# Kernel optimization log

Hardware: AMD Instinct MI355X
Metric: run time of the kernel (lower is better)

## Reference

```python
import jax, jax.numpy as jnp
import numpy as np

ROI = (8, 8)          # local window (kh, kw)
H = 768
W = 768
C = ROI[0] * ROI[1]   # 64 channels == prod(roi), required by the local conv
N_LAYERS = 4          # n_decoder_layers
LN_EPS = 1e-6         # flax.linen.LayerNorm default


def setup_inputs() -> dict:
    key = jax.random.key(0)
    k0, k1, k2 = jax.random.split(key, 3)
    x = jax.random.normal(k0, (H, W, C), jnp.float32)  # post-FPN feature map
    Ws = jax.random.normal(k1, (N_LAYERS, C, C), jnp.float32) / np.float32(np.sqrt(C))
    bs = jnp.zeros((N_LAYERS, C), jnp.float32)
    ln_scale = jnp.ones((N_LAYERS, C), jnp.float32)
    ln_bias = jnp.zeros((N_LAYERS, C), jnp.float32)
    w_out = jax.random.normal(k2, (C, 1), jnp.float32) / np.float32(np.sqrt(C))
    b_out = jnp.zeros((1,), jnp.float32)
    return {"x": x, "Ws": Ws, "bs": bs, "ln_scale": ln_scale,
            "ln_bias": ln_bias, "w_out": w_out, "b_out": b_out}


def att(x, weights):
    # out[i,j,c] = sum_{di,dj} xpad[i+di, j+dj, c] * weights[i, j, di*kw+dj]
    # Equivalent to the original per-channel lax.scan over
    # conv_general_dilated_local (window ordering row-major, 'same' padding),
    # but batched over all C channels at once via shifted-slice accumulation
    # instead of materializing the (H, W, 64, C) patch tensor.
    kh, kw = ROI
    pt, pb = (kh - 1) // 2, kh - 1 - (kh - 1) // 2  # 'SAME' pad for even kernel: (3, 4)
    pl, pr = (kw - 1) // 2, kw - 1 - (kw - 1) // 2
    xpad = jnp.pad(x, ((pt, pb), (pl, pr), (0, 0)))

    def body(acc, k):
        di = k // kw
        dj = k % kw
        patch = jax.lax.dynamic_slice(xpad, (di, dj, 0), (H, W, C))
        return acc + patch * weights[:, :, k][:, :, None], None

    acc, _ = jax.lax.scan(body, jnp.zeros_like(x), jnp.arange(kh * kw))
    return acc


def layer_norm(x, scale, bias):
    mu = jnp.mean(x, axis=-1, keepdims=True)
    var = jnp.mean(jnp.square(x - mu), axis=-1, keepdims=True)
    return (x - mu) * jax.lax.rsqrt(var + LN_EPS) * scale + bias


def reference(x, Ws, bs, ln_scale, ln_bias, w_out, b_out):
    weights = jax.nn.sigmoid(x)            # spatially-varying local-conv weights
    x0 = att(x, weights)                   # (H, W, C)
    for i in range(N_LAYERS):              # MLP decoder stack
        x0 = jax.nn.relu(x0 @ Ws[i] + bs[i])
        x0 = layer_norm(x0, ln_scale[i], ln_bias[i])
    out = x0 @ w_out + b_out               # (H, W, 1)
    return (x0, out)
```

## Files before the change

### kernel.cpp

```cpp
#include <hip/hip_runtime.h>
#include <hip/hip_bf16.h>


#define HH 768
#define WW 768
#define HWPX (HH*WW)

typedef __attribute__((ext_vector_type(8))) short short8;
typedef __attribute__((ext_vector_type(8))) _Float16 half8;
typedef __attribute__((ext_vector_type(4))) float f32x4;

union hcvt { _Float16 h; ushort u; };
__device__ __forceinline__ ushort f2h(float f) { hcvt c; c.h = (_Float16)f; return c.u; }
__device__ __forceinline__ float sigmoidf(float v) { return 1.f / (1.f + __expf(-v)); }

__device__ __forceinline__ int goff(int row, int g) {
  return (row << 8) + (((g & ~7) | ((g ^ row) & 7)) << 3);
}
__device__ __forceinline__ int eoff(int row, int k) {
  const int g = k >> 3;
  return (row << 8) + (((g & ~7) | ((g ^ row) & 7)) << 3) + (k & 7);
}

__global__ __launch_bounds__(256, 2)
void att_k1(const float* __restrict__ x, float* __restrict__ attf) {
  __shared__ __align__(16) ushort Mb[64 * 256];
  __shared__ __align__(16) ushort Xb[64 * 256];
  const int tid = threadIdx.x;
  const int lane = tid & 63, w = tid >> 6;
  const int l15 = lane & 15, lg = lane >> 4;

  {
    const short8 z8 = {0,0,0,0,0,0,0,0};
    #pragma unroll
    for (int i = 0; i < 8; ++i)
      *reinterpret_cast<short8*>(&Mb[(tid + i * 256) * 8]) = z8;
    if (tid < 128) {
      const int row = tid >> 1, g = 30 + (tid & 1);
      *reinterpret_cast<short8*>(&Xb[goff(row, g)]) = z8;
    }
  }

  const int b = blockIdx.x;
  const int tbase = (b & 7) * 1152 + (b >> 3) * 18;
  const int p  = w * 16 + l15;
  const int pr = p >> 3, pc = p & 7;
  const int cb = lg << 4;
  const int arow = w * 16 + l15;

  float4 cv[4];
  float Rv[4][8];
  float Lv[4][8];
  short8 rs[4];

  auto issue_loads = [&](int ti, int tj, bool fresh) {
    {
      const float* cp = x + ((size_t)((ti + pr) * WW + (tj + pc)) << 6) + cb;
      #pragma unroll
      for (int qd = 0; qd < 4; ++qd)
        cv[qd] = *reinterpret_cast<const float4*>(cp + qd * 4);
    }
    #pragma unroll
    for (int i = 0; i < 4; ++i) {
      const int r = w + 4 * i;
      if (r < 15) {
        const int gr = min(max(ti + r - 3, 0), HH - 1);
        const float* rowp = x + ((size_t)gr * WW << 6) + lane;
        #pragma unroll
        for (int s = 0; s < 8; ++s) {
          const int gc = min(max(tj + 5 + s, 0), WW - 1);
          Rv[i][s] = rowp[(size_t)gc << 6];
        }
        if (fresh) {
          #pragma unroll
          for (int s = 0; s < 8; ++s) {
            const int gc = min(max(tj - 3 + s, 0), WW - 1);
            Lv[i][s] = rowp[(size_t)gc << 6];
          }
        }
      }
    }
  };

  auto write_lds = [&](int ti, int tj, bool fresh) {
    #pragma unroll
    for (int qd = 0; qd < 4; ++qd) {
      const float vs[4] = {cv[qd].x, cv[qd].y, cv[qd].z, cv[qd].w};
      #pragma unroll
      for (int j = 0; j < 4; ++j) {
        const int ch = cb + qd * 4 + j;
        const int k = ((pr + (ch >> 3)) << 4) | (pc + (ch & 7));
        Mb[eoff(p, k)] = f2h(sigmoidf(vs[j]));
      }
    }
    #pragma unroll
    for (int i = 0; i < 4; ++i) {
      const int r = w + 4 * i;
      if (r < 15) {
        const int gr = ti + r - 3;
        const bool rok = (unsigned)gr < (unsigned)HH;
        short8 left8;
        if (fresh) {
          #pragma unroll
          for (int s = 0; s < 8; ++s) {
            const int j = tj - 3 + s;
            const bool ok = rok && ((unsigned)j < (unsigned)WW);
            left8[s] = (short)f2h(ok ? Lv[i][s] : 0.f);
          }
        } else {
          left8 = rs[i];
        }
        short8 right8;
        #pragma unroll
        for (int s = 0; s < 8; ++s) {
          const int j = tj + 5 + s;
          const bool ok = rok && ((unsigned)j < (unsigned)WW);
          right8[s] = (short)f2h(ok ? Rv[i][s] : 0.f);
        }
        *reinterpret_cast<short8*>(&Xb[goff(lane, 2 * r)])     = left8;
        *reinterpret_cast<short8*>(&Xb[goff(lane, 2 * r + 1)]) = right8;
        rs[i] = right8;
      }
    }
  };

  {
    const int t0 = tbase;
    issue_loads((t0 / 96) * 8, (t0 % 96) * 8, true);
  }

  for (int t18 = 0; t18 < 18; ++t18) {
    const int tile = tbase + t18;
    const int ti = (tile / 96) * 8, tj = (tile % 96) * 8;
    const bool fresh = (t18 == 0) || (tj == 0);

    __syncthreads();
    write_lds(ti, tj, fresh);
    __syncthreads();

    if (t18 < 17) {
      const int nt = tile + 1;
      issue_loads((nt / 96) * 8, (nt % 96) * 8, (nt % 96) == 0);
    }

    f32x4 acc[4];
    #pragma unroll
    for (int nb = 0; nb < 4; ++nb) acc[nb] = {0.f, 0.f, 0.f, 0.f};
    #pragma unroll
    for (int ks = 0; ks < 8; ++ks) {
      const int g = ks * 4 + lg;
      const half8 a = *reinterpret_cast<const half8*>(&Mb[goff(arow, g)]);
      #pragma unroll
      for (int nb = 0; nb < 4; ++nb) {
        const half8 bb = *reinterpret_cast<const half8*>(&Xb[goff(nb * 16 + l15, g)]);
        acc[nb] = __builtin_amdgcn_mfma_f32_16x16x32_f16(a, bb, acc[nb], 0, 0, 0);
      }
    }

    #pragma unroll
    for (int reg = 0; reg < 4; ++reg) {
      const int pl = w * 16 + lg * 4 + reg;
      const size_t gpx = (size_t)(ti + (pl >> 3)) * WW + (tj + (pl & 7));
      #pragma unroll
      for (int nb = 0; nb < 4; ++nb)
        attf[(gpx << 6) + nb * 16 + l15] = acc[nb][reg];
    }
  }
}

__global__ __launch_bounds__(512, 4)
void mlp_k2(const float* attf, const float* __restrict__ Ws,
            const float* __restrict__ bs, const float* __restrict__ lns,
            const float* __restrict__ lnb, const float* __restrict__ w_out,
            const float* __restrict__ b_out, float* x0_out,
            float* __restrict__ out1) {
  __shared__ __align__(16) ushort wt[4 * 64 * 64];
  __shared__ __align__(16) ushort act[8 * 1152];
  const int tid = threadIdx.x;
  const int lane = tid & 63, wid = tid >> 6;
  const int l15 = lane & 15, lg = lane >> 4;

  {
    const int row = tid >> 1;
    const int l = row >> 6, co = row & 63;
    const int ci0 = (tid & 1) << 5;
    const int base = row << 6;
    for (int q = 0; q < 32; ++q) {
      const int ci = ci0 + q;
      const float v = Ws[(((l << 6) + ci) << 6) + co];
      const int e = ((((ci >> 3) ^ co) & 7) << 3) | (ci & 7);
      wt[base + e] = f2h(v);
    }
  }
  float bias[4][4], sc[4][4], lbv[4][4];
  #pragma unroll
  for (int L = 0; L < 4; ++L)
    #pragma unroll
    for (int nb = 0; nb < 4; ++nb) {
      const int ch = (L << 6) + nb * 16 + l15;
      bias[L][nb] = bs[ch]; sc[L][nb] = lns[ch]; lbv[L][nb] = lnb[ch];
    }
  float wo[4];
  #pragma unroll
  for (int nb = 0; nb < 4; ++nb) wo[nb] = w_out[nb * 16 + l15];
  const float b0s = b_out[0];
  __syncthreads();

  ushort* const acth = act + wid * 1152;

  for (int it = 0; it < 18; ++it) {
    const int chunk = blockIdx.x + (it << 8);
    const int px_base = chunk * 128 + wid * 16;

    half8 a0, a1;
    {
      const float* ap = attf + ((size_t)(px_base + l15) << 6) + lg * 8;
      const float4 f0 = *reinterpret_cast<const float4*>(ap);
      const float4 f1 = *reinterpret_cast<const float4*>(ap + 4);
      const float4 f2 = *reinterpret_cast<const float4*>(ap + 32);
      const float4 f3 = *reinterpret_cast<const float4*>(ap + 36);
      a0[0]=(_Float16)f0.x; a0[1]=(_Float16)f0.y; a0[2]=(_Float16)f0.z; a0[3]=(_Float16)f0.w;
      a0[4]=(_Float16)f1.x; a0[5]=(_Float16)f1.y; a0[6]=(_Float16)f1.z; a0[7]=(_Float16)f1.w;
      a1[0]=(_Float16)f2.x; a1[1]=(_Float16)f2.y; a1[2]=(_Float16)f2.z; a1[3]=(_Float16)f2.w;
      a1[4]=(_Float16)f3.x; a1[5]=(_Float16)f3.y; a1[6]=(_Float16)f3.z; a1[7]=(_Float16)f3.w;
    }

    float y[4][4];
    #pragma unroll
    for (int layer = 0; layer < 4; ++layer) {
      if (layer > 0) {
        a0 = *reinterpret_cast<const half8*>(&acth[l15 * 72 + lg * 8]);
        a1 = *reinterpret_cast<const half8*>(&acth[l15 * 72 + 32 + lg * 8]);
      }
      f32x4 z[4];
      #pragma unroll
      for (int nb = 0; nb < 4; ++nb) {
        const int co = nb * 16 + l15;
        const int wb = ((layer << 6) + co) << 6;
        const int e0 = (((lg    ) ^ co) & 7) << 3;
        const int e1 = (((lg + 4) ^ co) & 7) << 3;
        const half8 b0 = *reinterpret_cast<const half8*>(&wt[wb + e0]);
        const half8 b1 = *reinterpret_cast<const half8*>(&wt[wb + e1]);
        z[nb] = {0.f, 0.f, 0.f, 0.f};
        z[nb] = __builtin_amdgcn_mfma_f32_16x16x32_f16(a0, b0, z[nb], 0, 0, 0);
        z[nb] = __builtin_amdgcn_mfma_f32_16x16x32_f16(a1, b1, z[nb], 0, 0, 0);
      }
      #pragma unroll
      for (int reg = 0; reg < 4; ++reg) {
        float s = 0.f, ss = 0.f;
        #pragma unroll
        for (int nb = 0; nb < 4; ++nb) {
          float v = z[nb][reg] + bias[layer][nb];
          v = fmaxf(v, 0.f);
          y[reg][nb] = v;
          s += v; ss += v * v;
        }
        #pragma unroll
        for (int m = 1; m <= 8; m <<= 1) { s += __shfl_xor(s, m, 64); ss += __shfl_xor(ss, m, 64); }
        const float mu = s * 0.015625f;
        const float var = ss * 0.015625f - mu * mu;
        const float rstd = rsqrtf(var + 1e-6f);
        #pragma unroll
        for (int nb = 0; nb < 4; ++nb)
          y[reg][nb] = (y[reg][nb] - mu) * rstd * sc[layer][nb] + lbv[layer][nb];
      }
      if (layer < 3) {
        #pragma unroll
        for (int reg = 0; reg < 4; ++reg) {
          const int row = lg * 4 + reg;
          #pragma unroll
          for (int nb = 0; nb < 4; ++nb)
            acth[row * 72 + nb * 16 + l15] = f2h(y[reg][nb]);
        }
      }
    }

    #pragma unroll
    for (int reg = 0; reg < 4; ++reg) {
      const size_t pxg = (size_t)px_base + lg * 4 + reg;
      #pragma unroll
      for (int nb = 0; nb < 4; ++nb)
        x0_out[(pxg << 6) + nb * 16 + l15] = y[reg][nb];
      float part = y[reg][0] * wo[0] + y[reg][1] * wo[1] + y[reg][2] * wo[2] + y[reg][3] * wo[3];
      #pragma unroll
      for (int m = 1; m <= 8; m <<= 1) part += __shfl_xor(part, m, 64);
      if (l15 == 0) out1[pxg] = part + b0s;
    }
  }
}

extern "C" void kernel_launch(void* const* d_in, const int* in_sizes, int n_in,
                              void* d_out, int out_size, void* d_ws, size_t ws_size,
                              hipStream_t stream) {
  const float* x     = (const float*)d_in[0];
  const float* Ws    = (const float*)d_in[1];
  const float* bs    = (const float*)d_in[2];
  const float* lns   = (const float*)d_in[3];
  const float* lnbv  = (const float*)d_in[4];
  const float* w_out = (const float*)d_in[5];
  const float* b_out = (const float*)d_in[6];
  float* x0_out = (float*)d_out;
  float* out1   = x0_out + (size_t)HWPX * 64;

  float* attbuf = (ws_size >= (size_t)HWPX * 64 * sizeof(float))
                      ? (float*)d_ws : (float*)d_out;

  att_k1<<<512, 256, 0, stream>>>(x, attbuf);
  mlp_k2<<<256, 512, 0, stream>>>((const float*)attbuf, Ws, bs, lns, lnbv,
                                  w_out, b_out, x0_out, out1);
}
```

Measured before the change: 222.3 us.

## Store attention intermediate as fp16, switch to 32x32 MFMA, defer stores

The attention kernel now writes its intermediate buffer as fp16 instead of fp32 when workspace allows. The MLP kernel reads those half8 values directly, which halves the intermediate traffic and removes conversion work. The attention matmul moves from 16x16x32 MFMAs to 32x32x16 MFMAs. It runs 15 k-steps split across two accumulators, dropping the padding zero columns that previously needed zeroing, and writes each tile's results during the next tile's iteration to overlap the stores with loads. Rounding the intermediate to fp16 adds a small precision loss, although the MLP already converted it to fp16 on input.

```diff
diff --git a/kernel.cpp b/kernel.cpp
--- a/kernel.cpp
+++ b/kernel.cpp
@@ -9,6 +9,7 @@
 typedef __attribute__((ext_vector_type(8))) short short8;
 typedef __attribute__((ext_vector_type(8))) _Float16 half8;
 typedef __attribute__((ext_vector_type(4))) float f32x4;
+typedef __attribute__((ext_vector_type(16))) float f32x16;
 
 union hcvt { _Float16 h; ushort u; };
 __device__ __forceinline__ ushort f2h(float f) { hcvt c; c.h = (_Float16)f; return c.u; }
@@ -22,23 +23,21 @@
   return (row << 8) + (((g & ~7) | ((g ^ row) & 7)) << 3) + (k & 7);
 }
 
+template<bool F16OUT>
 __global__ __launch_bounds__(256, 2)
-void att_k1(const float* __restrict__ x, float* __restrict__ attf) {
+void att_k1(const float* __restrict__ x, void* __restrict__ attout) {
   __shared__ __align__(16) ushort Mb[64 * 256];
   __shared__ __align__(16) ushort Xb[64 * 256];
   const int tid = threadIdx.x;
   const int lane = tid & 63, w = tid >> 6;
   const int l15 = lane & 15, lg = lane >> 4;
+  const int l31 = lane & 31, lh = lane >> 5;
 
   {
     const short8 z8 = {0,0,0,0,0,0,0,0};
     #pragma unroll
     for (int i = 0; i < 8; ++i)
       *reinterpret_cast<short8*>(&Mb[(tid + i * 256) * 8]) = z8;
-    if (tid < 128) {
-      const int row = tid >> 1, g = 30 + (tid & 1);
-      *reinterpret_cast<short8*>(&Xb[goff(row, g)]) = z8;
-    }
   }
 
   const int b = blockIdx.x;
@@ -46,7 +45,7 @@
   const int p  = w * 16 + l15;
   const int pr = p >> 3, pc = p & 7;
   const int cb = lg << 4;
-  const int arow = w * 16 + l15;
+  const int pb = w >> 1, cb2 = w & 1;
 
   float4 cv[4];
   float Rv[4][8];
@@ -124,10 +123,23 @@
     }
   };
 
-  {
-    const int t0 = tbase;
-    issue_loads((t0 / 96) * 8, (t0 % 96) * 8, true);
-  }
+  f32x16 acc0, acc1;
+  int pti = 0, ptj = 0;
+
+  auto store_acc = [&](int ti, int tj) {
+    #pragma unroll
+    for (int reg = 0; reg < 16; ++reg) {
+      const float v = acc0[reg] + acc1[reg];
+      const int prow = (reg & 3) + 8 * (reg >> 2) + 4 * lh;
+      const int p2 = pb * 32 + prow;
+      const size_t gpx = (size_t)(ti + (p2 >> 3)) * WW + (tj + (p2 & 7));
+      const int ch = cb2 * 32 + l31;
+      if (F16OUT) ((ushort*)attout)[(gpx << 6) + ch] = f2h(v);
+      else        ((float*)attout)[(gpx << 6) + ch] = v;
+    }
+  };
+
+  issue_loads((tbase / 96) * 8, (tbase % 96) * 8, true);
 
   for (int t18 = 0; t18 < 18; ++t18) {
     const int tile = tbase + t18;
@@ -138,38 +150,30 @@
     write_lds(ti, tj, fresh);
     __syncthreads();
 
+    if (t18 > 0) store_acc(pti, ptj);
     if (t18 < 17) {
       const int nt = tile + 1;
       issue_loads((nt / 96) * 8, (nt % 96) * 8, (nt % 96) == 0);
     }
 
-    f32x4 acc[4];
-    #pragma unroll
-    for (int nb = 0; nb < 4; ++nb) acc[nb] = {0.f, 0.f, 0.f, 0.f};
-    #pragma unroll
-    for (int ks = 0; ks < 8; ++ks) {
-      const int g = ks * 4 + lg;
-      const half8 a = *reinterpret_cast<const half8*>(&Mb[goff(arow, g)]);
-      #pragma unroll
-      for (int nb = 0; nb < 4; ++nb) {
-        const half8 bb = *reinterpret_cast<const half8*>(&Xb[goff(nb * 16 + l15, g)]);
-        acc[nb] = __builtin_amdgcn_mfma_f32_16x16x32_f16(a, bb, acc[nb], 0, 0, 0);
-      }
-    }
-
-    #pragma unroll
-    for (int reg = 0; reg < 4; ++reg) {
-      const int pl = w * 16 + lg * 4 + reg;
-      const size_t gpx = (size_t)(ti + (pl >> 3)) * WW + (tj + (pl & 7));
-      #pragma unroll
-      for (int nb = 0; nb < 4; ++nb)
-        attf[(gpx << 6) + nb * 16 + l15] = acc[nb][reg];
-    }
-  }
-}
-
+    acc0 = (f32x16){0,0,0,0,0,0,0,0,0,0,0,0,0,0,0,0};
+    acc1 = (f32x16){0,0,0,0,0,0,0,0,0,0,0,0,0,0,0,0};
+    #pragma unroll
+    for (int ks = 0; ks < 15; ++ks) {
+      const int g = 2 * ks + lh;
+      const half8 a  = *reinterpret_cast<const half8*>(&Mb[goff(pb * 32 + l31, g)]);
+      const half8 bb = *reinterpret_cast<const half8*>(&Xb[goff(cb2 * 32 + l31, g)]);
+      if (ks & 1) acc1 = __builtin_amdgcn_mfma_f32_32x32x16_f16(a, bb, acc1, 0, 0, 0);
+      else        acc0 = __builtin_amdgcn_mfma_f32_32x32x16_f16(a, bb, acc0, 0, 0, 0);
+    }
+    pti = ti; ptj = tj;
+  }
+  store_acc(pti, ptj);
+}
+
+template<bool F16IN>
 __global__ __launch_bounds__(512, 4)
-void mlp_k2(const float* attf, const float* __restrict__ Ws,
+void mlp_k2(const void* attv, const float* __restrict__ Ws,
             const float* __restrict__ bs, const float* __restrict__ lns,
             const float* __restrict__ lnb, const float* __restrict__ w_out,
             const float* __restrict__ b_out, float* x0_out,
@@ -213,8 +217,12 @@
     const int px_base = chunk * 128 + wid * 16;
 
     half8 a0, a1;
-    {
-      const float* ap = attf + ((size_t)(px_base + l15) << 6) + lg * 8;
+    if (F16IN) {
+      const ushort* ap = (const ushort*)attv + ((size_t)(px_base + l15) << 6) + lg * 8;
+      a0 = *reinterpret_cast<const half8*>(ap);
+      a1 = *reinterpret_cast<const half8*>(ap + 32);
+    } else {
+      const float* ap = (const float*)attv + ((size_t)(px_base + l15) << 6) + lg * 8;
       const float4 f0 = *reinterpret_cast<const float4*>(ap);
       const float4 f1 = *reinterpret_cast<const float4*>(ap + 4);
       const float4 f2 = *reinterpret_cast<const float4*>(ap + 32);
@@ -302,10 +310,14 @@
   float* x0_out = (float*)d_out;
   float* out1   = x0_out + (size_t)HWPX * 64;
 
-  float* attbuf = (ws_size >= (size_t)HWPX * 64 * sizeof(float))
-                      ? (float*)d_ws : (float*)d_out;
-
-  att_k1<<<512, 256, 0, stream>>>(x, attbuf);
-  mlp_k2<<<256, 512, 0, stream>>>((const float*)attbuf, Ws, bs, lns, lnbv,
-                                  w_out, b_out, x0_out, out1);
-}
+  if (ws_size >= (size_t)HWPX * 64 * sizeof(ushort)) {
+    ushort* atth = (ushort*)d_ws;
+    att_k1<true><<<512, 256, 0, stream>>>(x, atth);
+    mlp_k2<true><<<256, 512, 0, stream>>>(atth, Ws, bs, lns, lnbv,
+                                          w_out, b_out, x0_out, out1);
+  } else {
+    att_k1<false><<<512, 256, 0, stream>>>(x, d_out);
+    mlp_k2<false><<<256, 512, 0, stream>>>(d_out, Ws, bs, lns, lnbv,
+                                           w_out, b_out, x0_out, out1);
+  }
+}
```

After: 195.7 us. 11.9% less time.
